# Kernel optimization log

Measured on AMD Instinct MI355X. Metric: run time of the kernel, lower is better.

## Reference

```python
import jax, jax.numpy as jnp
import numpy as np

EMBED_DIM = 1024
NUM_HEADS = 16
HEAD_DIM = EMBED_DIM // NUM_HEADS


def setup_inputs() -> dict:
    key = jax.random.key(0)
    ks = jax.random.split(key, 12)
    B, Nq, Nkv, D = 4, 1024, 1024, EMBED_DIM
    s = 1.0 / np.sqrt(D)
    return {
        "query": jax.random.normal(ks[0], (B, Nq, D), jnp.float32),
        "key_value": jax.random.normal(ks[1], (B, Nkv, D), jnp.float32),
        "Wq": jax.random.normal(ks[2], (D, D), jnp.float32) * s,
        "bq": jnp.zeros((D,), jnp.float32),
        "Wk": jax.random.normal(ks[3], (D, D), jnp.float32) * s,
        "bk": jnp.zeros((D,), jnp.float32),
        "Wv": jax.random.normal(ks[4], (D, D), jnp.float32) * s,
        "bv": jnp.zeros((D,), jnp.float32),
        "Wo": jax.random.normal(ks[5], (D, D), jnp.float32) * s,
        "bo": jnp.zeros((D,), jnp.float32),
        "gamma": jnp.ones((D,), jnp.float32),
        "beta": jnp.zeros((D,), jnp.float32),
    }


def reference(query, key_value, Wq, bq, Wk, bk, Wv, bv, Wo, bo, gamma, beta):
    B, Nq, D = query.shape
    Nkv = key_value.shape[1]
    H, Hd = NUM_HEADS, HEAD_DIM
    # projections -> [B, H, N, Hd]
    q = (query @ Wq + bq).reshape(B, Nq, H, Hd).transpose(0, 2, 1, 3)
    k = (key_value @ Wk + bk).reshape(B, Nkv, H, Hd).transpose(0, 2, 1, 3)
    v = (key_value @ Wv + bv).reshape(B, Nkv, H, Hd).transpose(0, 2, 1, 3)
    scores = jnp.einsum("bhqd,bhkd->bhqk", q, k) / jnp.sqrt(jnp.float32(Hd))
    attn = jax.nn.softmax(scores, axis=-1)  # dropout = identity at eval
    out = jnp.einsum("bhqk,bhkd->bhqd", attn, v)
    out = out.transpose(0, 2, 1, 3).reshape(B, Nq, D)
    out = out @ Wo + bo
    # residual + LayerNorm (eps = 1e-5, torch default)
    x = query + out
    mu = jnp.mean(x, axis=-1, keepdims=True)
    var = jnp.mean(jnp.square(x - mu), axis=-1, keepdims=True)
    return (x - mu) / jnp.sqrt(var + 1e-5) * gamma + beta
```

## Files before the change

kernel.cpp:

```cpp
#include <hip/hip_runtime.h>

typedef unsigned short u16;
typedef unsigned int u32;
typedef __attribute__((ext_vector_type(2))) unsigned int u32x2;
typedef __attribute__((ext_vector_type(4))) unsigned short u16x4;
typedef __attribute__((ext_vector_type(8))) short short8;
typedef __attribute__((ext_vector_type(4))) float f32x4;

#define MFMA16(a, b, c) __builtin_amdgcn_mfma_f32_16x16x32_bf16(a, b, c, 0, 0, 0)

__device__ __forceinline__ u16 f2bf(float f) {
  unsigned u = __builtin_bit_cast(unsigned, f);
  u += 0x7fffu + ((u >> 16) & 1u);
  return (u16)(u >> 16);
}

__device__ __forceinline__ float bf2f(u16 b) {
  return __builtin_bit_cast(float, ((u32)b) << 16);
}

__device__ __forceinline__ u32 cvtpk(float lo, float hi) {
  u32 r;
  asm("v_cvt_pk_bf16_f32 %0, %1, %2" : "=v"(r) : "v"(lo), "v"(hi));
  return r;
}

__device__ __forceinline__ float ex2(float x) {
  float r;
  asm("v_exp_f32 %0, %1" : "=v"(r) : "v"(x));
  return r;
}

__device__ __forceinline__ void gl_lds16(const void* g, void* l) {
  __builtin_amdgcn_global_load_lds((const __attribute__((address_space(1))) char*)g,
                                   (__attribute__((address_space(3))) char*)l, 16, 0, 0);
}

__global__ __launch_bounds__(256) void cvt2_k(const float* __restrict__ a,
                                              const float* __restrict__ b,
                                              u16* __restrict__ oa, u16* __restrict__ ob) {
  const int bid = blockIdx.x;
  const float* in = (bid < 4096) ? a : b;
  u16* out = (bid < 4096) ? oa : ob;
  int i = (bid & 4095) * 256 + threadIdx.x;
  float4 v = ((const float4*)in)[i];
  u16x4 o;
  o.x = f2bf(v.x); o.y = f2bf(v.y); o.z = f2bf(v.z); o.w = f2bf(v.w);
  ((u16x4*)out)[i] = o;
}

__global__ __launch_bounds__(256) void wt_k(const float* __restrict__ W0, const float* __restrict__ W1,
                                            const float* __restrict__ W2, const float* __restrict__ W3,
                                            u16* __restrict__ T0, u16* __restrict__ T1,
                                            u16* __restrict__ T2, u16* __restrict__ T3) {
  const float* W; u16* T;
  switch (blockIdx.z) {
    case 0: W = W0; T = T0; break;
    case 1: W = W1; T = T1; break;
    case 2: W = W2; T = T2; break;
    default: W = W3; T = T3; break;
  }
  __shared__ __align__(16) u16 t[64][72];
  const int k0 = blockIdx.y * 64, n0 = blockIdx.x * 64;
  const int tid = threadIdx.x;
  const int r = tid >> 4, c4 = (tid & 15) * 4;
#pragma unroll
  for (int i = 0; i < 4; i++) {
    float4 v = *(const float4*)(W + (k0 + r + i * 16) * 1024 + n0 + c4);
    u16x4 o;
    o.x = f2bf(v.x); o.y = f2bf(v.y); o.z = f2bf(v.z); o.w = f2bf(v.w);
    *(u16x4*)&t[r + i * 16][c4] = o;
  }
  __syncthreads();
#pragma unroll
  for (int i = 0; i < 4; i++) {
    int nr = r + i * 16;
    u16x4 o;
    o.x = t[c4 + 0][nr]; o.y = t[c4 + 1][nr]; o.z = t[c4 + 2][nr]; o.w = t[c4 + 3][nr];
    *(u16x4*)(T + (n0 + nr) * 1024 + k0 + c4) = o;
  }
}

__global__ __launch_bounds__(256, 3) void gemmqkv_k(
    const u16* __restrict__ qbf, const u16* __restrict__ kvbf,
    const u16* __restrict__ Wqt, const u16* __restrict__ Wkt, const u16* __restrict__ Wvt,
    const float* __restrict__ pbq, const float* __restrict__ pbk, const float* __restrict__ pbv,
    u16* __restrict__ Qh, u16* __restrict__ Kh, u16* __restrict__ Vth) {
  const int lin = blockIdx.x;
  const int swz = (lin & 7) * 96 + (lin >> 3);
  const int x = swz & 7, y = (swz >> 3) & 31, z = swz >> 8;

  const u16* A  = (z == 0) ? qbf : kvbf;
  const u16* Bt = (z == 0) ? Wqt : (z == 1 ? Wkt : Wvt);
  const float* bias = (z == 0) ? pbq : (z == 1 ? pbk : pbv);

  __shared__ __align__(16) u16 As[128 * 64];
  __shared__ __align__(16) u16 Bs[128 * 64];
  const int tid = threadIdx.x;
  const int l = tid & 63, w = tid >> 6;
  const int lr = l >> 4, lc = l & 15;
  const int wr = w >> 1, wc = w & 1;
  const int m0 = y * 128, n0 = x * 128;

  f32x4 acc[4][4] = {};

  const int sr = tid >> 2, sc = (tid & 3) * 8;
  const u16* Ag = A + (m0 + sr) * 1024 + sc;
  const u16* Bg = Bt + (n0 + sr) * 1024 + sc;

  for (int k0 = 0; k0 < 1024; k0 += 64) {
    __syncthreads();
    gl_lds16(Ag + k0, As + tid * 8);
    gl_lds16(Ag + 64 * 1024 + k0, As + 2048 + tid * 8);
    gl_lds16(Bg + k0, Bs + tid * 8);
    gl_lds16(Bg + 64 * 1024 + k0, Bs + 2048 + tid * 8);
    gl_lds16(Ag + k0 + 32, As + 4096 + tid * 8);
    gl_lds16(Ag + 64 * 1024 + k0 + 32, As + 6144 + tid * 8);
    gl_lds16(Bg + k0 + 32, Bs + 4096 + tid * 8);
    gl_lds16(Bg + 64 * 1024 + k0 + 32, Bs + 6144 + tid * 8);
    __syncthreads();
    const u16* PA = (z == 2) ? Bs : As;
    const u16* PB = (z == 2) ? As : Bs;
    short8 af[4][2], bf[4][2];
    const int ks8 = lr * 8;
#pragma unroll
    for (int m = 0; m < 4; m++)
#pragma unroll
      for (int h = 0; h < 2; h++)
        af[m][h] = *(const short8*)(PA + h * 4096 + (wr * 64 + m * 16 + lc) * 32 + ks8);
#pragma unroll
    for (int n = 0; n < 4; n++)
#pragma unroll
      for (int h = 0; h < 2; h++)
        bf[n][h] = *(const short8*)(PB + h * 4096 + (wc * 64 + n * 16 + lc) * 32 + ks8);
#pragma unroll
    for (int m = 0; m < 4; m++)
#pragma unroll
      for (int n = 0; n < 4; n++) {
        acc[m][n] = MFMA16(af[m][0], bf[n][0], acc[m][n]);
        acc[m][n] = MFMA16(af[m][1], bf[n][1], acc[m][n]);
      }
  }

  if (z == 2) {
#pragma unroll
    for (int m = 0; m < 4; m++) {
#pragma unroll
      for (int r = 0; r < 4; r++) {
        int ncol = n0 + wr * 64 + m * 16 + lr * 4 + r;
        float bb = bias[ncol];
        int h = ncol >> 6, d = ncol & 63;
#pragma unroll
        for (int n = 0; n < 4; n++) {
          int tok = m0 + wc * 64 + n * 16 + lc;
          Vth[(((tok >> 10) * 16 + h) * 64 + d) * 1024 + (tok & 1023)] =
              f2bf(acc[m][n][r] + bb);
        }
      }
    }
  } else {
    u16* outb = (z == 0) ? Qh : Kh;
    const float scale = (z == 0) ? 0.18033688f : 1.0f;
#pragma unroll
    for (int m = 0; m < 4; m++)
#pragma unroll
      for (int n = 0; n < 4; n++) {
        int ncol = n0 + wc * 64 + n * 16 + lc;
        float bb = bias[ncol];
        int h = ncol >> 6, d = ncol & 63;
#pragma unroll
        for (int r = 0; r < 4; r++) {
          int tok = m0 + wr * 64 + m * 16 + lr * 4 + r;
          outb[(((tok >> 10) * 16 + h) * 1024 + (tok & 1023)) * 64 + d] =
              f2bf((acc[m][n][r] + bb) * scale);
        }
      }
  }
}

__global__ __launch_bounds__(256, 4) void gemmo_k(const u16* __restrict__ A,
                                                  const u16* __restrict__ Bt,
                                                  const float* __restrict__ bias,
                                                  u16* __restrict__ outb) {
  const int lin = blockIdx.x;
  const int swz = (lin & 7) * 64 + (lin >> 3);
  const int x = swz & 15, y = swz >> 4;

  __shared__ __align__(16) u16 As[128 * 64];
  __shared__ __align__(16) u16 Bs[64 * 64];
  const int tid = threadIdx.x;
  const int l = tid & 63, w = tid >> 6;
  const int lr = l >> 4, lc = l & 15;
  const int wr = w >> 1, wc = w & 1;
  const int m0 = y * 128, n0 = x * 64;

  f32x4 acc[4][2] = {};
  const int sc = (tid & 3) * 8;
  const u16* Ag = A + (m0 + (tid >> 2)) * 1024 + sc;
  const u16* Bg = Bt + (n0 + (tid >> 2)) * 1024 + sc;

  for (int k0 = 0; k0 < 1024; k0 += 64) {
    __syncthreads();
    gl_lds16(Ag + k0, As + tid * 8);
    gl_lds16(Ag + 64 * 1024 + k0, As + 2048 + tid * 8);
    gl_lds16(Bg + k0, Bs + tid * 8);
    gl_lds16(Ag + k0 + 32, As + 4096 + tid * 8);
    gl_lds16(Ag + 64 * 1024 + k0 + 32, As + 6144 + tid * 8);
    gl_lds16(Bg + k0 + 32, Bs + 2048 + tid * 8);
    __syncthreads();
    short8 af[4][2], bf[2][2];
    const int ks8 = lr * 8;
#pragma unroll
    for (int m = 0; m < 4; m++)
#pragma unroll
      for (int h = 0; h < 2; h++)
        af[m][h] = *(const short8*)(As + h * 4096 + (wr * 64 + m * 16 + lc) * 32 + ks8);
#pragma unroll
    for (int n = 0; n < 2; n++)
#pragma unroll
      for (int h = 0; h < 2; h++)
        bf[n][h] = *(const short8*)(Bs + h * 2048 + (wc * 32 + n * 16 + lc) * 32 + ks8);
#pragma unroll
    for (int m = 0; m < 4; m++)
#pragma unroll
      for (int n = 0; n < 2; n++) {
        acc[m][n] = MFMA16(af[m][0], bf[n][0], acc[m][n]);
        acc[m][n] = MFMA16(af[m][1], bf[n][1], acc[m][n]);
      }
  }
#pragma unroll
  for (int m = 0; m < 4; m++)
#pragma unroll
    for (int n = 0; n < 2; n++) {
      int ncol = n0 + wc * 32 + n * 16 + lc;
      float bb = bias[ncol];
#pragma unroll
      for (int r = 0; r < 4; r++) {
        int tok = m0 + wr * 64 + m * 16 + lr * 4 + r;
        outb[tok * 1024 + ncol] = f2bf(acc[m][n][r] + bb);
      }
    }
}

__global__ __launch_bounds__(256, 2) void attn_k(const u16* __restrict__ Q,
                                                 const u16* __restrict__ K,
                                                 const u16* __restrict__ Vt,
                                                 u16* __restrict__ O) {
  const int bid = blockIdx.x;
  const int xcd = bid & 7, j = bid >> 3;
  const int bh = xcd + 8 * (j & 7);
  const int q0 = (j >> 3) * 128;
  const int tid = threadIdx.x;
  const int w = tid >> 6, l = tid & 63;
  const int lr = l >> 4, lc = l & 15;
  const u16* Qh = Q + bh * (1024 * 64);
  const u16* Kh = K + bh * (1024 * 64);
  const u16* Vh = Vt + bh * (64 * 1024);

  __shared__ __align__(16) u16 Ks[2][64 * 64];
  __shared__ __align__(16) u16 Vs[2][64 * 64];
  __shared__ __align__(16) u32 Plds[4][2][16][32];

  const int st_row = tid >> 3;
  const int st_cb = (tid & 7) * 16;
  const int sw1 = (st_cb ^ ((st_row & 7) << 4)) >> 1;
  const int st_row2 = st_row + 32;
  const int sw2 = (st_cb ^ ((st_row2 & 7) << 4)) >> 1;

  const short8 ones = {0x3F80, 0x3F80, 0x3F80, 0x3F80, 0x3F80, 0x3F80, 0x3F80, 0x3F80};

  short8 bq[2][2];
#pragma unroll
  for (int g = 0; g < 2; g++)
#pragma unroll
    for (int ks = 0; ks < 2; ks++)
      bq[g][ks] = *(const short8*)(Qh + (q0 + w * 32 + g * 16 + lc) * 64 + ks * 32 + lr * 8);

  f32x4 oacc[2][4] = {};
  f32x4 sacc[2] = {};
  float mrun[2] = {-1e30f, -1e30f};

  gl_lds16(Kh + st_row * 64 + sw1, &Ks[0][tid * 8]);
  gl_lds16(Kh + st_row2 * 64 + sw2, &Ks[0][2048 + tid * 8]);
  gl_lds16(Vh + st_row * 1024 + sw1, &Vs[0][tid * 8]);
  gl_lds16(Vh + st_row2 * 1024 + sw2, &Vs[0][2048 + tid * 8]);

  const int xw = (lc & 7) << 2;

  for (int t = 0; t < 16; ++t) {
    const int pb = t & 1;
    if (t < 15) {
      const int kvn = (t + 1) * 64;
      gl_lds16(Kh + (kvn + st_row) * 64 + sw1, &Ks[pb ^ 1][tid * 8]);
      gl_lds16(Kh + (kvn + st_row2) * 64 + sw2, &Ks[pb ^ 1][2048 + tid * 8]);
      gl_lds16(Vh + st_row * 1024 + kvn + sw1, &Vs[pb ^ 1][tid * 8]);
      gl_lds16(Vh + st_row2 * 1024 + kvn + sw2, &Vs[pb ^ 1][2048 + tid * 8]);
      asm volatile("s_waitcnt vmcnt(4)" ::: "memory");
    } else {
      asm volatile("s_waitcnt vmcnt(0)" ::: "memory");
    }
    __builtin_amdgcn_s_barrier();
    asm volatile("" ::: "memory");

    const u16* Kb = Ks[pb];
    const u16* Vb = Vs[pb];

    f32x4 s0[4] = {}, s1[4] = {};
    __builtin_amdgcn_s_setprio(1);
#pragma unroll
    for (int mk = 0; mk < 4; mk++) {
      const int krow = mk * 16 + lc;
      const u16* kp = Kb + krow * 64;
#pragma unroll
      for (int ks = 0; ks < 2; ks++) {
        const int cb = (ks * 64 + lr * 16) ^ ((krow & 7) << 4);
        short8 ak = *(const short8*)(kp + (cb >> 1));
        s0[mk] = MFMA16(ak, bq[0][ks], s0[mk]);
        s1[mk] = MFMA16(ak, bq[1][ks], s1[mk]);
      }
    }
    __builtin_amdgcn_s_setprio(0);

    float mx0, mx1;
    {
      float a = fmaxf(fmaxf(s0[0][0], s0[0][1]), fmaxf(s0[0][2], s0[0][3]));
      float b = fmaxf(fmaxf(s0[1][0], s0[1][1]), fmaxf(s0[1][2], s0[1][3]));
      float c = fmaxf(fmaxf(s0[2][0], s0[2][1]), fmaxf(s0[2][2], s0[2][3]));
      float d = fmaxf(fmaxf(s0[3][0], s0[3][1]), fmaxf(s0[3][2], s0[3][3]));
      mx0 = fmaxf(fmaxf(a, b), fmaxf(c, d));
      float e = fmaxf(fmaxf(s1[0][0], s1[0][1]), fmaxf(s1[0][2], s1[0][3]));
      float f = fmaxf(fmaxf(s1[1][0], s1[1][1]), fmaxf(s1[1][2], s1[1][3]));
      float g2 = fmaxf(fmaxf(s1[2][0], s1[2][1]), fmaxf(s1[2][2], s1[2][3]));
      float h = fmaxf(fmaxf(s1[3][0], s1[3][1]), fmaxf(s1[3][2], s1[3][3]));
      mx1 = fmaxf(fmaxf(e, f), fmaxf(g2, h));
    }

    if (!__all(mx0 <= mrun[0] + 8.f && mx1 <= mrun[1] + 8.f)) {
      mx0 = fmaxf(mx0, __shfl_xor(mx0, 16));
      mx0 = fmaxf(mx0, __shfl_xor(mx0, 32));
      mx1 = fmaxf(mx1, __shfl_xor(mx1, 16));
      mx1 = fmaxf(mx1, __shfl_xor(mx1, 32));
      float mn0 = fmaxf(mrun[0], mx0), mn1 = fmaxf(mrun[1], mx1);
      float al0 = ex2(mrun[0] - mn0), al1 = ex2(mrun[1] - mn1);
      mrun[0] = mn0; mrun[1] = mn1;
      float a0[4], a1[4];
#pragma unroll
      for (int r = 0; r < 4; r++) {
        a0[r] = __shfl(al0, lr * 4 + r);
        a1[r] = __shfl(al1, lr * 4 + r);
      }
#pragma unroll
      for (int r = 0; r < 4; r++) {
        sacc[0][r] *= a0[r];
        sacc[1][r] *= a1[r];
      }
#pragma unroll
      for (int nd = 0; nd < 4; nd++)
#pragma unroll
        for (int r = 0; r < 4; r++) {
          oacc[0][nd][r] *= a0[r];
          oacc[1][nd][r] *= a1[r];
        }
    }

#pragma unroll
    for (int mk = 0; mk < 4; mk++)
#pragma unroll
      for (int r = 0; r < 4; r++) {
        s0[mk][r] = ex2(s0[mk][r] - mrun[0]);
        s1[mk][r] = ex2(s1[mk][r] - mrun[1]);
      }

    u32* PW0 = &Plds[w][0][lc][0];
    u32* PW1 = &Plds[w][1][lc][0];
#pragma unroll
    for (int mk = 0; mk < 4; mk++) {
      const int idx = (mk * 8 + lr * 2) ^ xw;
      u32x2 p0 = {cvtpk(s0[mk][0], s0[mk][1]), cvtpk(s0[mk][2], s0[mk][3])};
      u32x2 p1 = {cvtpk(s1[mk][0], s1[mk][1]), cvtpk(s1[mk][2], s1[mk][3])};
      *(u32x2*)&PW0[idx] = p0;
      *(u32x2*)&PW1[idx] = p1;
    }

    __builtin_amdgcn_s_setprio(1);
#pragma unroll
    for (int ks = 0; ks < 2; ks++) {
      short8 ap0 = *(const short8*)&Plds[w][0][lc][(ks * 16 + lr * 4) ^ xw];
      short8 ap1 = *(const short8*)&Plds[w][1][lc][(ks * 16 + lr * 4) ^ xw];
      sacc[0] = MFMA16(ap0, ones, sacc[0]);
      sacc[1] = MFMA16(ap1, ones, sacc[1]);
#pragma unroll
      for (int nd = 0; nd < 4; nd++) {
        const int vrow = nd * 16 + lc;
        const int cb = (ks * 64 + lr * 16) ^ ((vrow & 7) << 4);
        short8 bv = *(const short8*)(Vb + vrow * 64 + (cb >> 1));
        oacc[0][nd] = MFMA16(ap0, bv, oacc[0][nd]);
        oacc[1][nd] = MFMA16(ap1, bv, oacc[1][nd]);
      }
    }
    __builtin_amdgcn_s_setprio(0);

    asm volatile("" ::: "memory");
    __builtin_amdgcn_s_barrier();
  }

  const int b = bh >> 4, h = bh & 15;
#pragma unroll
  for (int g = 0; g < 2; g++) {
    float invr[4];
#pragma unroll
    for (int r = 0; r < 4; r++) invr[r] = 1.f / sacc[g][r];
#pragma unroll
    for (int r = 0; r < 4; r++) {
      int row = b * 1024 + q0 + w * 32 + g * 16 + lr * 4 + r;
#pragma unroll
      for (int nd = 0; nd < 4; nd++)
        O[row * 1024 + h * 64 + nd * 16 + lc] = f2bf(oacc[g][nd][r] * invr[r]);
    }
  }
}

__global__ __launch_bounds__(256) void ln_k(const float* __restrict__ q,
                                            const u16* __restrict__ p2,
                                            const float* __restrict__ gamma,
                                            const float* __restrict__ beta,
                                            float* __restrict__ out) {
  const int row = blockIdx.x, tid = threadIdx.x;
  float4 xq = ((const float4*)(q + row * 1024))[tid];
  u16x4 xpb = ((const u16x4*)(p2 + row * 1024))[tid];
  float4 x = {xq.x + bf2f(xpb.x), xq.y + bf2f(xpb.y),
              xq.z + bf2f(xpb.z), xq.w + bf2f(xpb.w)};
  float s = x.x + x.y + x.z + x.w;
#pragma unroll
  for (int off = 1; off < 64; off <<= 1) s += __shfl_xor(s, off);
  __shared__ float red[8];
  const int w = tid >> 6;
  if ((tid & 63) == 0) red[w] = s;
  __syncthreads();
  float mu = (red[0] + red[1] + red[2] + red[3]) * (1.0f / 1024.0f);
  float4 dx = {x.x - mu, x.y - mu, x.z - mu, x.w - mu};
  float s2 = dx.x * dx.x + dx.y * dx.y + dx.z * dx.z + dx.w * dx.w;
#pragma unroll
  for (int off = 1; off < 64; off <<= 1) s2 += __shfl_xor(s2, off);
  if ((tid & 63) == 0) red[4 + w] = s2;
  __syncthreads();
  float var = (red[4] + red[5] + red[6] + red[7]) * (1.0f / 1024.0f);
  float rs = rsqrtf(var + 1e-5f);
  float4 g = ((const float4*)gamma)[tid];
  float4 bb = ((const float4*)beta)[tid];
  float4 o = {dx.x * rs * g.x + bb.x, dx.y * rs * g.y + bb.y,
              dx.z * rs * g.z + bb.z, dx.w * rs * g.w + bb.w};
  ((float4*)(out + row * 1024))[tid] = o;
}

extern "C" void kernel_launch(void* const* d_in, const int* in_sizes, int n_in,
                              void* d_out, int out_size, void* d_ws, size_t ws_size,
                              hipStream_t stream) {
  const float* query = (const float*)d_in[0];
  const float* kv    = (const float*)d_in[1];
  const float* Wq = (const float*)d_in[2];
  const float* bq = (const float*)d_in[3];
  const float* Wk = (const float*)d_in[4];
  const float* bk = (const float*)d_in[5];
  const float* Wv = (const float*)d_in[6];
  const float* bv = (const float*)d_in[7];
  const float* Wo = (const float*)d_in[8];
  const float* bo = (const float*)d_in[9];
  const float* gamma = (const float*)d_in[10];
  const float* beta  = (const float*)d_in[11];
  float* out = (float*)d_out;

  char* ws = (char*)d_ws;
  const size_t MB = 1u << 20;
  u16* qbf  = (u16*)(ws + 0 * MB);
  u16* kvbf = (u16*)(ws + 8 * MB);
  u16* Wqt  = (u16*)(ws + 16 * MB);
  u16* Wkt  = (u16*)(ws + 18 * MB);
  u16* Wvt  = (u16*)(ws + 20 * MB);
  u16* Wot  = (u16*)(ws + 22 * MB);
  u16* Qh   = (u16*)(ws + 24 * MB);
  u16* Kh   = (u16*)(ws + 32 * MB);
  u16* Vth  = (u16*)(ws + 40 * MB);
  u16* attO = (u16*)(ws + 48 * MB);
  u16* p2b  = (u16*)(ws + 56 * MB);

  cvt2_k<<<dim3(8192), dim3(256), 0, stream>>>(query, kv, qbf, kvbf);
  wt_k<<<dim3(16, 16, 4), dim3(256), 0, stream>>>(Wq, Wk, Wv, Wo, Wqt, Wkt, Wvt, Wot);

  gemmqkv_k<<<dim3(768), dim3(256), 0, stream>>>(qbf, kvbf, Wqt, Wkt, Wvt,
                                                 bq, bk, bv, Qh, Kh, Vth);

  attn_k<<<dim3(512), dim3(256), 0, stream>>>(Qh, Kh, Vth, attO);

  gemmo_k<<<dim3(512), dim3(256), 0, stream>>>(attO, Wot, bo, p2b);

  ln_k<<<dim3(4096), dim3(256), 0, stream>>>(query, p2b, gamma, beta, out);
}
```

Measured before the change: 99.85 us.

## Software-pipeline the attention PV matmul one KV tile behind the QK step

The P·V MFMA block for KV tile t-1 now runs at the start of iteration t, before the next K/V prefetch and the QK MFMAs for tile t. A trailing epilogue handles the last tile. The P staging buffer in LDS is double-buffered so probabilities from the previous tile survive while new ones are written. The aim is to let the exp/softmax work of one tile overlap with matrix work of another and to hide barrier latency, at the cost of extra LDS and a reordered barrier and prefetch schedule.

```diff
diff --git a/kernel.cpp b/kernel.cpp
--- a/kernel.cpp
+++ b/kernel.cpp
@@ -259,7 +259,7 @@
 
   __shared__ __align__(16) u16 Ks[2][64 * 64];
   __shared__ __align__(16) u16 Vs[2][64 * 64];
-  __shared__ __align__(16) u32 Plds[4][2][16][32];
+  __shared__ __align__(16) u32 Plds[2][4][2][16][32];
 
   const int st_row = tid >> 3;
   const int st_cb = (tid & 7) * 16;
@@ -289,6 +289,31 @@
 
   for (int t = 0; t < 16; ++t) {
     const int pb = t & 1;
+
+    if (t > 0) {
+      const u16* Vb = Vs[pb ^ 1];
+      __builtin_amdgcn_s_setprio(1);
+#pragma unroll
+      for (int ks = 0; ks < 2; ks++) {
+        short8 ap0 = *(const short8*)&Plds[pb ^ 1][w][0][lc][(ks * 16 + lr * 4) ^ xw];
+        short8 ap1 = *(const short8*)&Plds[pb ^ 1][w][1][lc][(ks * 16 + lr * 4) ^ xw];
+        sacc[0] = MFMA16(ap0, ones, sacc[0]);
+        sacc[1] = MFMA16(ap1, ones, sacc[1]);
+#pragma unroll
+        for (int nd = 0; nd < 4; nd++) {
+          const int vrow = nd * 16 + lc;
+          const int cb = (ks * 64 + lr * 16) ^ ((vrow & 7) << 4);
+          short8 bv = *(const short8*)(Vb + vrow * 64 + (cb >> 1));
+          oacc[0][nd] = MFMA16(ap0, bv, oacc[0][nd]);
+          oacc[1][nd] = MFMA16(ap1, bv, oacc[1][nd]);
+        }
+      }
+      __builtin_amdgcn_s_setprio(0);
+      asm volatile("" ::: "memory");
+      __builtin_amdgcn_s_barrier();
+      asm volatile("" ::: "memory");
+    }
+
     if (t < 15) {
       const int kvn = (t + 1) * 64;
       gl_lds16(Kh + (kvn + st_row) * 64 + sw1, &Ks[pb ^ 1][tid * 8]);
@@ -303,7 +328,6 @@
     asm volatile("" ::: "memory");
 
     const u16* Kb = Ks[pb];
-    const u16* Vb = Vs[pb];
 
     f32x4 s0[4] = {}, s1[4] = {};
     __builtin_amdgcn_s_setprio(1);
@@ -371,8 +395,8 @@
         s1[mk][r] = ex2(s1[mk][r] - mrun[1]);
       }
 
-    u32* PW0 = &Plds[w][0][lc][0];
-    u32* PW1 = &Plds[w][1][lc][0];
+    u32* PW0 = &Plds[pb][w][0][lc][0];
+    u32* PW1 = &Plds[pb][w][1][lc][0];
 #pragma unroll
     for (int mk = 0; mk < 4; mk++) {
       const int idx = (mk * 8 + lr * 2) ^ xw;
@@ -381,12 +405,15 @@
       *(u32x2*)&PW0[idx] = p0;
       *(u32x2*)&PW1[idx] = p1;
     }
-
+  }
+
+  {
+    const u16* Vb = Vs[1];
     __builtin_amdgcn_s_setprio(1);
 #pragma unroll
     for (int ks = 0; ks < 2; ks++) {
-      short8 ap0 = *(const short8*)&Plds[w][0][lc][(ks * 16 + lr * 4) ^ xw];
-      short8 ap1 = *(const short8*)&Plds[w][1][lc][(ks * 16 + lr * 4) ^ xw];
+      short8 ap0 = *(const short8*)&Plds[1][w][0][lc][(ks * 16 + lr * 4) ^ xw];
+      short8 ap1 = *(const short8*)&Plds[1][w][1][lc][(ks * 16 + lr * 4) ^ xw];
       sacc[0] = MFMA16(ap0, ones, sacc[0]);
       sacc[1] = MFMA16(ap1, ones, sacc[1]);
 #pragma unroll
@@ -399,9 +426,6 @@
       }
     }
     __builtin_amdgcn_s_setprio(0);
-
-    asm volatile("" ::: "memory");
-    __builtin_amdgcn_s_barrier();
   }
 
   const int b = bh >> 4, h = bh & 15;
```

Measured after the change: 100.6 us. About the same (+0.7%).

## Fuse K and V projections into one block sharing the key_value tile

Applied to the files above, without the earlier changes.

The QKV GEMM grid goes from 768 to 512 blocks. Q blocks compute only the Q projection, while K/V blocks load the key_value tile once and use it for both the K and V projections, with a second weight tile and accumulator set. This removes the duplicate load of key_value A tiles for the V projection. In exchange the work is unbalanced (K/V blocks do twice the MFMA work of Q blocks), LDS per block rises to 48KB, register pressure doubles, and launch bounds drop occupancy to 2 blocks.

```diff
diff --git a/kernel.cpp b/kernel.cpp
--- a/kernel.cpp
+++ b/kernel.cpp
@@ -81,21 +81,23 @@
   }
 }
 
-__global__ __launch_bounds__(256, 3) void gemmqkv_k(
+__global__ __launch_bounds__(256, 2) void gemmqkv_k(
     const u16* __restrict__ qbf, const u16* __restrict__ kvbf,
     const u16* __restrict__ Wqt, const u16* __restrict__ Wkt, const u16* __restrict__ Wvt,
     const float* __restrict__ pbq, const float* __restrict__ pbk, const float* __restrict__ pbv,
     u16* __restrict__ Qh, u16* __restrict__ Kh, u16* __restrict__ Vth) {
   const int lin = blockIdx.x;
-  const int swz = (lin & 7) * 96 + (lin >> 3);
-  const int x = swz & 7, y = (swz >> 3) & 31, z = swz >> 8;
-
-  const u16* A  = (z == 0) ? qbf : kvbf;
-  const u16* Bt = (z == 0) ? Wqt : (z == 1 ? Wkt : Wvt);
-  const float* bias = (z == 0) ? pbq : (z == 1 ? pbk : pbv);
+  const int t = (lin & 7) * 64 + (lin >> 3);
+  const int zz = t & 1;
+  const int u = t >> 1;
+  const int x = u & 7, y = u >> 3;
+
+  const u16* A  = zz ? kvbf : qbf;
+  const u16* Bt = zz ? Wkt : Wqt;
 
   __shared__ __align__(16) u16 As[128 * 64];
   __shared__ __align__(16) u16 Bs[128 * 64];
+  __shared__ __align__(16) u16 Cs[128 * 64];
   const int tid = threadIdx.x;
   const int l = tid & 63, w = tid >> 6;
   const int lr = l >> 4, lc = l & 15;
@@ -103,78 +105,119 @@
   const int m0 = y * 128, n0 = x * 128;
 
   f32x4 acc[4][4] = {};
+  f32x4 accv[4][4] = {};
 
   const int sr = tid >> 2, sc = (tid & 3) * 8;
   const u16* Ag = A + (m0 + sr) * 1024 + sc;
   const u16* Bg = Bt + (n0 + sr) * 1024 + sc;
+  const u16* Cg = Wvt + (n0 + sr) * 1024 + sc;
 
   for (int k0 = 0; k0 < 1024; k0 += 64) {
     __syncthreads();
     gl_lds16(Ag + k0, As + tid * 8);
     gl_lds16(Ag + 64 * 1024 + k0, As + 2048 + tid * 8);
+    gl_lds16(Ag + k0 + 32, As + 4096 + tid * 8);
+    gl_lds16(Ag + 64 * 1024 + k0 + 32, As + 6144 + tid * 8);
     gl_lds16(Bg + k0, Bs + tid * 8);
     gl_lds16(Bg + 64 * 1024 + k0, Bs + 2048 + tid * 8);
-    gl_lds16(Ag + k0 + 32, As + 4096 + tid * 8);
-    gl_lds16(Ag + 64 * 1024 + k0 + 32, As + 6144 + tid * 8);
     gl_lds16(Bg + k0 + 32, Bs + 4096 + tid * 8);
     gl_lds16(Bg + 64 * 1024 + k0 + 32, Bs + 6144 + tid * 8);
+    if (zz) {
+      gl_lds16(Cg + k0, Cs + tid * 8);
+      gl_lds16(Cg + 64 * 1024 + k0, Cs + 2048 + tid * 8);
+      gl_lds16(Cg + k0 + 32, Cs + 4096 + tid * 8);
+      gl_lds16(Cg + 64 * 1024 + k0 + 32, Cs + 6144 + tid * 8);
+    }
     __syncthreads();
-    const u16* PA = (z == 2) ? Bs : As;
-    const u16* PB = (z == 2) ? As : Bs;
-    short8 af[4][2], bf[4][2];
     const int ks8 = lr * 8;
+    {
+      short8 a0[4][2], b0[4][2];
+#pragma unroll
+      for (int m = 0; m < 4; m++)
+#pragma unroll
+        for (int h = 0; h < 2; h++)
+          a0[m][h] = *(const short8*)(As + h * 4096 + (wr * 64 + m * 16 + lc) * 32 + ks8);
+#pragma unroll
+      for (int n = 0; n < 4; n++)
+#pragma unroll
+        for (int h = 0; h < 2; h++)
+          b0[n][h] = *(const short8*)(Bs + h * 4096 + (wc * 64 + n * 16 + lc) * 32 + ks8);
+#pragma unroll
+      for (int m = 0; m < 4; m++)
+#pragma unroll
+        for (int n = 0; n < 4; n++) {
+          acc[m][n] = MFMA16(a0[m][0], b0[n][0], acc[m][n]);
+          acc[m][n] = MFMA16(a0[m][1], b0[n][1], acc[m][n]);
+        }
+    }
+    if (zz) {
+      short8 a1[4][2], b1[4][2];
+#pragma unroll
+      for (int m = 0; m < 4; m++)
+#pragma unroll
+        for (int h = 0; h < 2; h++)
+          a1[m][h] = *(const short8*)(Cs + h * 4096 + (wr * 64 + m * 16 + lc) * 32 + ks8);
+#pragma unroll
+      for (int n = 0; n < 4; n++)
+#pragma unroll
+        for (int h = 0; h < 2; h++)
+          b1[n][h] = *(const short8*)(As + h * 4096 + (wc * 64 + n * 16 + lc) * 32 + ks8);
+#pragma unroll
+      for (int m = 0; m < 4; m++)
+#pragma unroll
+        for (int n = 0; n < 4; n++) {
+          accv[m][n] = MFMA16(a1[m][0], b1[n][0], accv[m][n]);
+          accv[m][n] = MFMA16(a1[m][1], b1[n][1], accv[m][n]);
+        }
+    }
+  }
+
+  if (zz == 0) {
+    const float scale = 0.18033688f;
 #pragma unroll
     for (int m = 0; m < 4; m++)
 #pragma unroll
-      for (int h = 0; h < 2; h++)
-        af[m][h] = *(const short8*)(PA + h * 4096 + (wr * 64 + m * 16 + lc) * 32 + ks8);
-#pragma unroll
-    for (int n = 0; n < 4; n++)
-#pragma unroll
-      for (int h = 0; h < 2; h++)
-        bf[n][h] = *(const short8*)(PB + h * 4096 + (wc * 64 + n * 16 + lc) * 32 + ks8);
+      for (int n = 0; n < 4; n++) {
+        int ncol = n0 + wc * 64 + n * 16 + lc;
+        float bb = pbq[ncol];
+        int h = ncol >> 6, d = ncol & 63;
+#pragma unroll
+        for (int r = 0; r < 4; r++) {
+          int tok = m0 + wr * 64 + m * 16 + lr * 4 + r;
+          Qh[(((tok >> 10) * 16 + h) * 1024 + (tok & 1023)) * 64 + d] =
+              f2bf((acc[m][n][r] + bb) * scale);
+        }
+      }
+  } else {
 #pragma unroll
     for (int m = 0; m < 4; m++)
 #pragma unroll
       for (int n = 0; n < 4; n++) {
-        acc[m][n] = MFMA16(af[m][0], bf[n][0], acc[m][n]);
-        acc[m][n] = MFMA16(af[m][1], bf[n][1], acc[m][n]);
-      }
-  }
-
-  if (z == 2) {
+        int ncol = n0 + wc * 64 + n * 16 + lc;
+        float bb = pbk[ncol];
+        int h = ncol >> 6, d = ncol & 63;
+#pragma unroll
+        for (int r = 0; r < 4; r++) {
+          int tok = m0 + wr * 64 + m * 16 + lr * 4 + r;
+          Kh[(((tok >> 10) * 16 + h) * 1024 + (tok & 1023)) * 64 + d] =
+              f2bf(acc[m][n][r] + bb);
+        }
+      }
 #pragma unroll
     for (int m = 0; m < 4; m++) {
 #pragma unroll
       for (int r = 0; r < 4; r++) {
         int ncol = n0 + wr * 64 + m * 16 + lr * 4 + r;
-        float bb = bias[ncol];
+        float bb = pbv[ncol];
         int h = ncol >> 6, d = ncol & 63;
 #pragma unroll
         for (int n = 0; n < 4; n++) {
           int tok = m0 + wc * 64 + n * 16 + lc;
           Vth[(((tok >> 10) * 16 + h) * 64 + d) * 1024 + (tok & 1023)] =
-              f2bf(acc[m][n][r] + bb);
+              f2bf(accv[m][n][r] + bb);
         }
       }
     }
-  } else {
-    u16* outb = (z == 0) ? Qh : Kh;
-    const float scale = (z == 0) ? 0.18033688f : 1.0f;
-#pragma unroll
-    for (int m = 0; m < 4; m++)
-#pragma unroll
-      for (int n = 0; n < 4; n++) {
-        int ncol = n0 + wc * 64 + n * 16 + lc;
-        float bb = bias[ncol];
-        int h = ncol >> 6, d = ncol & 63;
-#pragma unroll
-        for (int r = 0; r < 4; r++) {
-          int tok = m0 + wr * 64 + m * 16 + lr * 4 + r;
-          outb[(((tok >> 10) * 16 + h) * 1024 + (tok & 1023)) * 64 + d] =
-              f2bf((acc[m][n][r] + bb) * scale);
-        }
-      }
   }
 }
 
@@ -487,7 +530,7 @@
   cvt2_k<<<dim3(8192), dim3(256), 0, stream>>>(query, kv, qbf, kvbf);
   wt_k<<<dim3(16, 16, 4), dim3(256), 0, stream>>>(Wq, Wk, Wv, Wo, Wqt, Wkt, Wvt, Wot);
 
-  gemmqkv_k<<<dim3(768), dim3(256), 0, stream>>>(qbf, kvbf, Wqt, Wkt, Wvt,
+  gemmqkv_k<<<dim3(512), dim3(256), 0, stream>>>(qbf, kvbf, Wqt, Wkt, Wvt,
                                                  bq, bk, bv, Qh, Kh, Vth);
 
   attn_k<<<dim3(512), dim3(256), 0, stream>>>(Qh, Kh, Vth, attO);
```

Result: slower. 104.6 us (+4.8%).

## Load V tiles directly from global into registers instead of staging through LDS

Applied to the files above, without the earlier changes.

The attention kernel stops double-buffering V in shared memory. Each wave now issues global_load_dwordx4 for its V fragments at the start of each KV iteration and waits on them just before the PV MFMAs. This cuts LDS footprint and LDS read traffic for V, but every wave now fetches V redundantly from global/L2 with latency exposed in the same iteration. It also depends on hand-tuned vmcnt counts.

```diff
diff --git a/kernel.cpp b/kernel.cpp
--- a/kernel.cpp
+++ b/kernel.cpp
@@ -34,6 +34,12 @@
 __device__ __forceinline__ void gl_lds16(const void* g, void* l) {
   __builtin_amdgcn_global_load_lds((const __attribute__((address_space(1))) char*)g,
                                    (__attribute__((address_space(3))) char*)l, 16, 0, 0);
+}
+
+__device__ __forceinline__ short8 ldg16(const u16* p) {
+  f32x4 r;
+  asm volatile("global_load_dwordx4 %0, %1, off" : "=v"(r) : "v"(p));
+  return __builtin_bit_cast(short8, r);
 }
 
 __global__ __launch_bounds__(256) void cvt2_k(const float* __restrict__ a,
@@ -258,7 +264,6 @@
   const u16* Vh = Vt + bh * (64 * 1024);
 
   __shared__ __align__(16) u16 Ks[2][64 * 64];
-  __shared__ __align__(16) u16 Vs[2][64 * 64];
   __shared__ __align__(16) u32 Plds[4][2][16][32];
 
   const int st_row = tid >> 3;
@@ -280,30 +285,36 @@
   f32x4 sacc[2] = {};
   float mrun[2] = {-1e30f, -1e30f};
 
+  const u16* vb0 = Vh + lc * 1024 + lr * 8;
+
   gl_lds16(Kh + st_row * 64 + sw1, &Ks[0][tid * 8]);
   gl_lds16(Kh + st_row2 * 64 + sw2, &Ks[0][2048 + tid * 8]);
-  gl_lds16(Vh + st_row * 1024 + sw1, &Vs[0][tid * 8]);
-  gl_lds16(Vh + st_row2 * 1024 + sw2, &Vs[0][2048 + tid * 8]);
 
   const int xw = (lc & 7) << 2;
 
   for (int t = 0; t < 16; ++t) {
     const int pb = t & 1;
+    const int kv0 = t * 64;
+
+    short8 vreg[8];
+#pragma unroll
+    for (int ks = 0; ks < 2; ks++)
+#pragma unroll
+      for (int nd = 0; nd < 4; nd++)
+        vreg[ks * 4 + nd] = ldg16(vb0 + nd * 16 * 1024 + kv0 + ks * 32);
+
     if (t < 15) {
-      const int kvn = (t + 1) * 64;
+      const int kvn = kv0 + 64;
       gl_lds16(Kh + (kvn + st_row) * 64 + sw1, &Ks[pb ^ 1][tid * 8]);
       gl_lds16(Kh + (kvn + st_row2) * 64 + sw2, &Ks[pb ^ 1][2048 + tid * 8]);
-      gl_lds16(Vh + st_row * 1024 + kvn + sw1, &Vs[pb ^ 1][tid * 8]);
-      gl_lds16(Vh + st_row2 * 1024 + kvn + sw2, &Vs[pb ^ 1][2048 + tid * 8]);
-      asm volatile("s_waitcnt vmcnt(4)" ::: "memory");
+      asm volatile("s_waitcnt vmcnt(10)" ::: "memory");
     } else {
-      asm volatile("s_waitcnt vmcnt(0)" ::: "memory");
+      asm volatile("s_waitcnt vmcnt(8)" ::: "memory");
     }
     __builtin_amdgcn_s_barrier();
     asm volatile("" ::: "memory");
 
     const u16* Kb = Ks[pb];
-    const u16* Vb = Vs[pb];
 
     f32x4 s0[4] = {}, s1[4] = {};
     __builtin_amdgcn_s_setprio(1);
@@ -382,6 +393,12 @@
       *(u32x2*)&PW1[idx] = p1;
     }
 
+    if (t < 15)
+      asm volatile("s_waitcnt vmcnt(2)" ::: "memory");
+    else
+      asm volatile("s_waitcnt vmcnt(0)" ::: "memory");
+    __builtin_amdgcn_sched_barrier(0);
+
     __builtin_amdgcn_s_setprio(1);
 #pragma unroll
     for (int ks = 0; ks < 2; ks++) {
@@ -391,9 +408,7 @@
       sacc[1] = MFMA16(ap1, ones, sacc[1]);
 #pragma unroll
       for (int nd = 0; nd < 4; nd++) {
-        const int vrow = nd * 16 + lc;
-        const int cb = (ks * 64 + lr * 16) ^ ((vrow & 7) << 4);
-        short8 bv = *(const short8*)(Vb + vrow * 64 + (cb >> 1));
+        short8 bv = vreg[ks * 4 + nd];
         oacc[0][nd] = MFMA16(ap0, bv, oacc[0][nd]);
         oacc[1][nd] = MFMA16(ap1, bv, oacc[1][nd]);
       }
```

Result: slower. 109.2 us (+9.4%).
